# Performance work log

Measured on AMD Instinct MI355X. Metric: run time of the kernel, lower is better.

Reference implementation:

```python
import jax, jax.numpy as jnp
import numpy as np

H, DH, M = 8, 64, 3          # heads, dim_head, num memory tokens
DIM = 512                    # model dim
INNER = H * DH               # 512
SCALE = DH ** -0.5
SQRT_DH = float(np.sqrt(DH))
SQRT_M = float(np.sqrt(M))


def setup_inputs() -> dict:
    key = jax.random.key(0)
    ks = jax.random.split(key, 7)
    b, n = 2, 2048
    x = jax.random.normal(ks[0], (b, n, DIM), dtype=jnp.float32)
    # Linear weights stored as (in, out); y = x @ W
    wq = jax.random.normal(ks[1], (DIM, INNER), dtype=jnp.float32) * (DIM ** -0.5)
    wkv = jax.random.normal(ks[2], (DIM, 2 * INNER), dtype=jnp.float32) * (DIM ** -0.5)
    wo = jax.random.normal(ks[3], (INNER, DIM), dtype=jnp.float32) * (INNER ** -0.5)
    bo = jnp.zeros((DIM,), dtype=jnp.float32)
    # xavier_normal_ std = sqrt(2 / (fan_in + fan_out)) over last two dims (M, INNER)
    xav = float(np.sqrt(2.0 / (M + INNER)))
    m_k = jax.random.normal(ks[4], (1, M, INNER), dtype=jnp.float32) * xav
    m_v = jax.random.normal(ks[5], (1, M, INNER), dtype=jnp.float32) * xav
    return {"x": x, "wq": wq, "wkv": wkv, "wo": wo, "bo": bo, "m_k": m_k, "m_v": m_v}


def reference(x, wq, wkv, wo, bo, m_k, m_v):
    b, n, _ = x.shape
    # projections -> (b, h, n, d)
    q = (x @ wq).reshape(b, n, H, DH).transpose(0, 2, 1, 3)
    kv = x @ wkv
    k, v = jnp.split(kv, 2, axis=-1)
    k = k.reshape(b, n, H, DH).transpose(0, 2, 1, 3)
    v = v.reshape(b, n, H, DH).transpose(0, 2, 1, 3)
    # memory tokens: torch does expand(b, M, INNER).view(b, H, M, DH),
    # a flat reshape (NOT a per-head rearrange) -- replicate exactly.
    mk = SQRT_DH * jnp.broadcast_to(m_k, (b, M, INNER)).reshape(b, H, M, DH)
    mv = SQRT_M * jnp.broadcast_to(m_v, (b, M, INNER)).reshape(b, H, M, DH)
    k = jnp.concatenate([k, mk], axis=2)  # (b, h, n+M, d)
    v = jnp.concatenate([v, mv], axis=2)
    dots = jnp.einsum('bhid,bhjd->bhij', q, k) * SCALE  # (b, h, n, n+M)
    attn = jax.nn.softmax(dots, axis=-1)                # dropout = identity (eval)
    out = jnp.einsum('bhij,bhjd->bhid', attn, v)
    out = out.transpose(0, 2, 1, 3).reshape(b, n, INNER)
    return out @ wo + bo
```

## Files before the change

### kernel.cpp

```cpp
#include <hip/hip_runtime.h>

typedef unsigned short u16;
typedef unsigned int u32;
typedef __attribute__((ext_vector_type(8))) __bf16 bf16x8;
typedef __attribute__((ext_vector_type(4))) float f32x4;

#define DEVI __device__ __forceinline__
#define C1 0.180336880f
#define C2 (-23.0831200f)

DEVI float bf2f(u16 u) {
    unsigned int v = ((unsigned int)u) << 16;
    return __uint_as_float(v);
}
DEVI u16 f2bf(float f) {
    unsigned int x = __float_as_uint(f);
    x += 0x7fffu + ((x >> 16) & 1u);
    return (u16)(x >> 16);
}
DEVI u32 pk2(float lo, float hi) {
    union { __bf16 b[2]; u32 u; } c;
    c.b[0] = (__bf16)lo; c.b[1] = (__bf16)hi;
    return c.u;
}
DEVI bf16x8 ldb8(const u16* p) {
    union { uint4 u; bf16x8 b; } c;
    c.u = *(const uint4*)p;
    return c.b;
}
DEVI f32x4 mfma32(bf16x8 a, bf16x8 b, f32x4 c) {
    return __builtin_amdgcn_mfma_f32_16x16x32_bf16(a, b, c, 0, 0, 0);
}
DEVI float clamp4(float v) { return fminf(fmaxf(v, -1e4f), 1e4f); }
DEVI float fexp2(float x) { return __builtin_amdgcn_exp2f(x); }
DEVI void gld16(const u16* g, u16* l) {
    __builtin_amdgcn_global_load_lds(
        (const __attribute__((address_space(1))) void*)g,
        (__attribute__((address_space(3))) void*)l, 16, 0, 0);
}

__global__ __launch_bounds__(256) void prep(
    const float* __restrict__ wq, const float* __restrict__ wkv,
    const float* __restrict__ wo, const float* __restrict__ x,
    const float* __restrict__ mkf, const float* __restrict__ mvf,
    u16* __restrict__ wqkvT, u16* __restrict__ woT, u16* __restrict__ xb,
    u16* __restrict__ qkv)
{
    const int bid = blockIdx.x, tid = threadIdx.x;
    if (bid < 256) {
        __shared__ u16 T[64][68];
        int j0, k0; const float* W; int ldw; u16* Out;
        if (bid < 192) { int jt = bid % 24, kt = bid / 24;
            j0 = jt * 64; k0 = kt * 64;
            if (j0 < 512) { W = wq + j0;          ldw = 512;  }
            else          { W = wkv + (j0 - 512); ldw = 1024; }
            Out = wqkvT;
        } else { int t = bid - 192;
            j0 = (t >> 3) * 64; k0 = (t & 7) * 64;
            W = wo + j0; ldw = 512; Out = woT;
        }
        const int lr = tid >> 4, lc = tid & 15;
        #pragma unroll
        for (int i = 0; i < 4; ++i) {
            int k = lr + i * 16;
            float4 v = *(const float4*)(W + (size_t)(k0 + k) * ldw + lc * 4);
            u16 p[4] = { f2bf(v.x), f2bf(v.y), f2bf(v.z), f2bf(v.w) };
            *(uint2*)&T[k][lc * 4] = *(uint2*)p;
        }
        __syncthreads();
        #pragma unroll
        for (int i = 0; i < 4; ++i) {
            int j = lr + i * 16;
            u16 p[4];
            #pragma unroll
            for (int c = 0; c < 4; ++c) p[c] = T[lc * 4 + c][j];
            *(uint2*)(Out + (size_t)(j0 + j) * 512 + k0 + lc * 4) = *(uint2*)p;
        }
    } else if (bid < 2304) {
        int e = (bid - 256) * 1024 + tid * 4;
        float4 v = *(const float4*)(x + e);
        u16 p[4] = { f2bf(v.x), f2bf(v.y), f2bf(v.z), f2bf(v.w) };
        *(uint2*)(xb + e) = *(uint2*)p;
    } else {
        int e = (bid - 2304) * 256 + tid;
        int b = e >> 16, rem = e & 65535;
        int row2 = rem >> 10, c = rem & 1023;
        float v = 0.f;
        if (row2 < 3) {
            int hh = (c & 511) >> 6, d = c & 63;
            int src = hh * 192 + row2 * 64 + d;
            v = (c < 512) ? 8.0f * mkf[src] : 1.7320508f * mvf[src];
        }
        qkv[((size_t)b * 2112 + 2048 + row2) * 1536 + 512 + c] = f2bf(v);
    }
}

template<int TM, int TN, bool F32OUT>
__global__ __launch_bounds__(256) void gemmK(
    const u16* __restrict__ A, int lda,
    const u16* __restrict__ BT, int ldb,
    void* __restrict__ Cv, int ldc,
    const float* __restrict__ bias, int K, int mpad)
{
    constexpr int IL = TM / 32, JL = TN / 32;
    __shared__ u16 As0[TM * 32], As1[TM * 32];
    __shared__ u16 Bs0[TN * 32], Bs1[TN * 32];

    const int tid = threadIdx.x;
    const int m0 = blockIdx.x * TM, n0 = blockIdx.y * TN;
    const int w = tid >> 6, lane = tid & 63, l15 = lane & 15, quad = lane >> 4;
    const int wr = w >> 1, wc = w & 1;
    const int sr = lane >> 2, sc = (lane & 3) * 8;

    f32x4 acc[IL][JL];
    #pragma unroll
    for (int i = 0; i < IL; ++i)
        #pragma unroll
        for (int j = 0; j < JL; ++j) acc[i][j] = (f32x4){0.f, 0.f, 0.f, 0.f};

    for (int k0 = 0; k0 < K; k0 += 64) {
        __syncthreads();
        #pragma unroll
        for (int p = 0; p < TM / 64; ++p) {
            int r0 = w * (TM / 4) + p * 16;
            const u16* g = A + (size_t)(m0 + r0 + sr) * lda + k0 + sc;
            gld16(g,      &As0[r0 * 32]);
            gld16(g + 32, &As1[r0 * 32]);
        }
        #pragma unroll
        for (int p = 0; p < TN / 64; ++p) {
            int r0 = w * (TN / 4) + p * 16;
            const u16* g = BT + (size_t)(n0 + r0 + sr) * ldb + k0 + sc;
            gld16(g,      &Bs0[r0 * 32]);
            gld16(g + 32, &Bs1[r0 * 32]);
        }
        __syncthreads();

        #pragma unroll
        for (int ks = 0; ks < 2; ++ks) {
            const u16* Asel = ks ? As1 : As0;
            const u16* Bsel = ks ? Bs1 : Bs0;
            bf16x8 af[IL], bf[JL];
            #pragma unroll
            for (int i = 0; i < IL; ++i)
                af[i] = ldb8(&Asel[(wr * (TM / 2) + 16 * i + l15) * 32 + quad * 8]);
            #pragma unroll
            for (int j = 0; j < JL; ++j)
                bf[j] = ldb8(&Bsel[(wc * (TN / 2) + 16 * j + l15) * 32 + quad * 8]);
            #pragma unroll
            for (int i = 0; i < IL; ++i)
                #pragma unroll
                for (int j = 0; j < JL; ++j)
                    acc[i][j] = mfma32(af[i], bf[j], acc[i][j]);
        }
    }

    #pragma unroll
    for (int j = 0; j < JL; ++j) {
        int col = n0 + wc * (TN / 2) + 16 * j + l15;
        float bv = bias ? bias[col] : 0.f;
        #pragma unroll
        for (int i = 0; i < IL; ++i) {
            #pragma unroll
            for (int r = 0; r < 4; ++r) {
                int row = m0 + wr * (TM / 2) + 16 * i + quad * 4 + r;
                int orow = row + ((row >> 11) * mpad);
                float vr = clamp4(acc[i][j][r] + bv);
                if (F32OUT) ((float*)Cv)[(size_t)orow * ldc + col] = vr;
                else        ((u16*)Cv)[(size_t)orow * ldc + col] = f2bf(vr);
            }
        }
    }
}

__global__ __launch_bounds__(256, 4) void attn_kernel(
    const u16* __restrict__ qkv, u16* __restrict__ Opart,
    float* __restrict__ Lpart)
{
    __shared__ alignas(16) u16 Ks[64][72];
    __shared__ alignas(16) u16 Vt[64][72];
    __shared__ alignas(16) u16 Ps[128][72];

    const int tid = threadIdx.x;
    const int bx = blockIdx.x;
    const int qt = bx >> 2, s = bx & 3;
    const int h = blockIdx.y, b = blockIdx.z;
    const int w = tid >> 6, lane = tid & 63, l15 = lane & 15, quad = lane >> 4;
    const size_t bq = (size_t)b * 2112;
    const int rq = qt * 128;
    const int ro = b * 2048 + qt * 128;

    union { u32 u[4]; bf16x8 b8; } onesu;
    #pragma unroll
    for (int i = 0; i < 4; ++i) onesu.u[i] = 0x3F803F80u;
    const bf16x8 onesf = onesu.b8;

    {
        int row = tid >> 1, cg = (tid & 1) * 32;
        const u16* src = qkv + (bq + rq + row) * 1536 + h * 64 + cg;
        *(uint4*)&Ps[row][cg]      = *(const uint4*)src;
        *(uint4*)&Ps[row][cg + 8]  = *(const uint4*)(src + 8);
        *(uint4*)&Ps[row][cg + 16] = *(const uint4*)(src + 16);
        *(uint4*)&Ps[row][cg + 24] = *(const uint4*)(src + 24);
    }
    __syncthreads();
    bf16x8 qf[2][2];
    #pragma unroll
    for (int sub = 0; sub < 2; ++sub) {
        qf[sub][0] = ldb8(&Ps[64 * sub + 16 * w + l15][quad * 8]);
        qf[sub][1] = ldb8(&Ps[64 * sub + 16 * w + l15][32 + quad * 8]);
    }

    f32x4 Od[2][4], Ol[2];
    #pragma unroll
    for (int sub = 0; sub < 2; ++sub) {
        #pragma unroll
        for (int t = 0; t < 4; ++t) Od[sub][t] = (f32x4){0.f, 0.f, 0.f, 0.f};
        Ol[sub] = (f32x4){0.f, 0.f, 0.f, 0.f};
    }

    const int krow = tid >> 2, kcg = (tid & 3) * 16;
    const int vkp = (tid & 31) * 2, vdg = ((tid >> 5) & 7) * 8;

    const int kt0 = s ? 8 * s + 1 : 0;
    const int kt1 = 8 * s + 9;
    for (int kt = kt0; kt < kt1; ++kt) {
        const u16* ksrc = qkv + (bq + kt * 64 + krow) * 1536 + 512 + h * 64 + kcg;
        uint4 k0 = *(const uint4*)ksrc, k1 = *(const uint4*)(ksrc + 8);
        const u16* vsrc = qkv + (bq + kt * 64 + vkp) * 1536 + 1024 + h * 64 + vdg;
        uint4 v0 = *(const uint4*)vsrc, v1 = *(const uint4*)(vsrc + 1536);
        __syncthreads();
        *(uint4*)&Ks[krow][kcg]     = k0;
        *(uint4*)&Ks[krow][kcg + 8] = k1;
        {
            u32 a0[4] = {v0.x, v0.y, v0.z, v0.w};
            u32 a1[4] = {v1.x, v1.y, v1.z, v1.w};
            #pragma unroll
            for (int i = 0; i < 4; ++i) {
                u32 lo = __builtin_amdgcn_perm(a1[i], a0[i], 0x05040100u);
                u32 hi = __builtin_amdgcn_perm(a1[i], a0[i], 0x07060302u);
                *(u32*)&Vt[vdg + 2 * i][vkp]     = lo;
                *(u32*)&Vt[vdg + 2 * i + 1][vkp] = hi;
            }
        }
        __syncthreads();

        f32x4 d[2][4];
        #pragma unroll
        for (int sub = 0; sub < 2; ++sub)
            #pragma unroll
            for (int t = 0; t < 4; ++t) d[sub][t] = (f32x4){0.f, 0.f, 0.f, 0.f};
        #pragma unroll
        for (int ks = 0; ks < 2; ++ks) {
            #pragma unroll
            for (int t = 0; t < 4; ++t) {
                bf16x8 kf = ldb8(&Ks[16 * t + l15][ks * 32 + quad * 8]);
                d[0][t] = mfma32(kf, qf[0][ks], d[0][t]);
                d[1][t] = mfma32(kf, qf[1][ks], d[1][t]);
            }
        }
        if (kt == 32) {
            #pragma unroll
            for (int sub = 0; sub < 2; ++sub) {
                #pragma unroll
                for (int t = 1; t < 4; ++t)
                    d[sub][t] = (f32x4){-1e9f, -1e9f, -1e9f, -1e9f};
                #pragma unroll
                for (int r = 0; r < 4; ++r)
                    if (!(quad == 0 && r < 3)) d[sub][0][r] = -1e9f;
            }
        }

        #pragma unroll
        for (int sub = 0; sub < 2; ++sub)
            #pragma unroll
            for (int t = 0; t < 4; ++t) {
                uint2 pv = { pk2(fexp2(fmaf(d[sub][t][0], C1, C2)),
                                 fexp2(fmaf(d[sub][t][1], C1, C2))),
                             pk2(fexp2(fmaf(d[sub][t][2], C1, C2)),
                                 fexp2(fmaf(d[sub][t][3], C1, C2))) };
                *(uint2*)&Ps[64 * sub + 16 * w + l15][16 * t + 4 * quad] = pv;
            }
        #pragma unroll
        for (int ks = 0; ks < 2; ++ks) {
            bf16x8 af0 = ldb8(&Ps[16 * w + l15][ks * 32 + quad * 8]);
            bf16x8 af1 = ldb8(&Ps[64 + 16 * w + l15][ks * 32 + quad * 8]);
            #pragma unroll
            for (int dt = 0; dt < 4; ++dt) {
                bf16x8 vf = ldb8(&Vt[16 * dt + l15][ks * 32 + quad * 8]);
                Od[0][dt] = mfma32(af0, vf, Od[0][dt]);
                Od[1][dt] = mfma32(af1, vf, Od[1][dt]);
            }
            Ol[0] = mfma32(af0, onesf, Ol[0]);
            Ol[1] = mfma32(af1, onesf, Ol[1]);
        }
    }

    u16* Ob = Opart + (size_t)s * 4096 * 512;
    #pragma unroll
    for (int sub = 0; sub < 2; ++sub) {
        #pragma unroll
        for (int r = 0; r < 4; ++r) {
            int row = ro + 64 * sub + 16 * w + quad * 4 + r;
            #pragma unroll
            for (int dt = 0; dt < 4; ++dt) {
                int col = h * 64 + 16 * dt + l15;
                Ob[(size_t)row * 512 + col] = f2bf(Od[sub][dt][r]);
            }
            if (l15 == 0)
                Lpart[((size_t)s * 4096 + row) * 8 + h] = Ol[sub][r];
        }
    }
}

__global__ __launch_bounds__(256) void merge_kernel(
    const u16* __restrict__ Opart, const float* __restrict__ Lpart,
    u16* __restrict__ outp)
{
    int e = (blockIdx.x * 256 + threadIdx.x) * 4;
    int row = e >> 9, h = (e & 511) >> 6;
    float ax = 0.f, ay = 0.f, az = 0.f, aw = 0.f, l = 0.f;
    #pragma unroll
    for (int s = 0; s < 4; ++s) {
        uint2 pv = *(const uint2*)(Opart + (size_t)s * 4096 * 512 + e);
        ax += bf2f((u16)(pv.x & 0xffff)); ay += bf2f((u16)(pv.x >> 16));
        az += bf2f((u16)(pv.y & 0xffff)); aw += bf2f((u16)(pv.y >> 16));
        l += Lpart[((size_t)s * 4096 + row) * 8 + h];
    }
    float rl = 1.0f / fmaxf(l, 1e-30f);
    u16 p[4] = { f2bf(clamp4(ax * rl)), f2bf(clamp4(ay * rl)),
                 f2bf(clamp4(az * rl)), f2bf(clamp4(aw * rl)) };
    *(uint2*)(outp + e) = *(uint2*)p;
}

extern "C" void kernel_launch(void* const* d_in, const int* in_sizes, int n_in,
                              void* d_out, int out_size, void* d_ws, size_t ws_size,
                              hipStream_t stream)
{
    (void)in_sizes; (void)n_in; (void)out_size; (void)ws_size;
    const float* x   = (const float*)d_in[0];
    const float* wq  = (const float*)d_in[1];
    const float* wkv = (const float*)d_in[2];
    const float* wo  = (const float*)d_in[3];
    const float* bo  = (const float*)d_in[4];
    const float* mk  = (const float*)d_in[5];
    const float* mv  = (const float*)d_in[6];
    float* out = (float*)d_out;

    u16* qkv   = (u16*)d_ws;
    u16* outp  = qkv + 6488064;
    u16* woT   = outp + 2097152;
    float* Lpart = (float*)(woT + 262144);
    u16* scratch = (u16*)(Lpart + 163840);
    u16* wqkvT = scratch;
    u16* xb    = scratch + 786432;
    u16* Opart = scratch;

    prep<<<2816, 256, 0, stream>>>(wq, wkv, wo, x, mk, mv, wqkvT, woT, xb, qkv);
    gemmK<128, 64, false><<<dim3(32, 24), 256, 0, stream>>>(
        xb, 512, wqkvT, 512, qkv, 1536, nullptr, 512, 64);
    attn_kernel<<<dim3(64, 8, 2), 256, 0, stream>>>(qkv, Opart, Lpart);
    merge_kernel<<<2048, 256, 0, stream>>>(Opart, Lpart, outp);
    gemmK<64, 64, true><<<dim3(64, 8), 256, 0, stream>>>(
        outp, 512, woT, 512, out, 512, bo, 512, 0);
}
```

Before: 129.7 us.

## Fuse split-KV merge into output projection GEMM and enlarge QKV GEMM K-tile

Removes the separate merge kernel: the output-projection GEMM now reads the four split-KV partial outputs and their softmax denominators, sums and normalizes them in registers, and writes the merged bf16 tile straight into shared memory as the A operand. This drops one launch and the write and re-read of the merged intermediate. The cost is that each of the 8 column-blocks repeats the 4-way partial reads and the reduction, which raises Opart traffic. Separately, the QKV GEMM is parameterized on K-tile depth and run with BK=128, halving its barrier iterations at the cost of more shared memory.

```diff
diff --git a/kernel.cpp b/kernel.cpp
--- a/kernel.cpp
+++ b/kernel.cpp
@@ -95,16 +95,16 @@
     }
 }
 
-template<int TM, int TN, bool F32OUT>
+template<int TM, int TN, int BK, bool F32OUT>
 __global__ __launch_bounds__(256) void gemmK(
     const u16* __restrict__ A, int lda,
     const u16* __restrict__ BT, int ldb,
     void* __restrict__ Cv, int ldc,
     const float* __restrict__ bias, int K, int mpad)
 {
-    constexpr int IL = TM / 32, JL = TN / 32;
-    __shared__ u16 As0[TM * 32], As1[TM * 32];
-    __shared__ u16 Bs0[TN * 32], Bs1[TN * 32];
+    constexpr int IL = TM / 32, JL = TN / 32, KS = BK / 32;
+    __shared__ u16 As[KS][TM * 32];
+    __shared__ u16 Bs[KS][TN * 32];
 
     const int tid = threadIdx.x;
     const int m0 = blockIdx.x * TM, n0 = blockIdx.y * TN;
@@ -118,35 +118,35 @@
         #pragma unroll
         for (int j = 0; j < JL; ++j) acc[i][j] = (f32x4){0.f, 0.f, 0.f, 0.f};
 
-    for (int k0 = 0; k0 < K; k0 += 64) {
+    for (int k0 = 0; k0 < K; k0 += BK) {
         __syncthreads();
         #pragma unroll
         for (int p = 0; p < TM / 64; ++p) {
             int r0 = w * (TM / 4) + p * 16;
             const u16* g = A + (size_t)(m0 + r0 + sr) * lda + k0 + sc;
-            gld16(g,      &As0[r0 * 32]);
-            gld16(g + 32, &As1[r0 * 32]);
+            #pragma unroll
+            for (int kk = 0; kk < KS; ++kk)
+                gld16(g + 32 * kk, &As[kk][r0 * 32]);
         }
         #pragma unroll
         for (int p = 0; p < TN / 64; ++p) {
             int r0 = w * (TN / 4) + p * 16;
             const u16* g = BT + (size_t)(n0 + r0 + sr) * ldb + k0 + sc;
-            gld16(g,      &Bs0[r0 * 32]);
-            gld16(g + 32, &Bs1[r0 * 32]);
-        }
-        __syncthreads();
-
-        #pragma unroll
-        for (int ks = 0; ks < 2; ++ks) {
-            const u16* Asel = ks ? As1 : As0;
-            const u16* Bsel = ks ? Bs1 : Bs0;
+            #pragma unroll
+            for (int kk = 0; kk < KS; ++kk)
+                gld16(g + 32 * kk, &Bs[kk][r0 * 32]);
+        }
+        __syncthreads();
+
+        #pragma unroll
+        for (int ks = 0; ks < KS; ++ks) {
             bf16x8 af[IL], bf[JL];
             #pragma unroll
             for (int i = 0; i < IL; ++i)
-                af[i] = ldb8(&Asel[(wr * (TM / 2) + 16 * i + l15) * 32 + quad * 8]);
+                af[i] = ldb8(&As[ks][(wr * (TM / 2) + 16 * i + l15) * 32 + quad * 8]);
             #pragma unroll
             for (int j = 0; j < JL; ++j)
-                bf[j] = ldb8(&Bsel[(wc * (TN / 2) + 16 * j + l15) * 32 + quad * 8]);
+                bf[j] = ldb8(&Bs[ks][(wc * (TN / 2) + 16 * j + l15) * 32 + quad * 8]);
             #pragma unroll
             for (int i = 0; i < IL; ++i)
                 #pragma unroll
@@ -313,24 +313,95 @@
     }
 }
 
-__global__ __launch_bounds__(256) void merge_kernel(
+__global__ __launch_bounds__(256) void gemm2f(
     const u16* __restrict__ Opart, const float* __restrict__ Lpart,
-    u16* __restrict__ outp)
+    const u16* __restrict__ BT, float* __restrict__ Cout,
+    const float* __restrict__ bias)
 {
-    int e = (blockIdx.x * 256 + threadIdx.x) * 4;
-    int row = e >> 9, h = (e & 511) >> 6;
-    float ax = 0.f, ay = 0.f, az = 0.f, aw = 0.f, l = 0.f;
-    #pragma unroll
-    for (int s = 0; s < 4; ++s) {
-        uint2 pv = *(const uint2*)(Opart + (size_t)s * 4096 * 512 + e);
-        ax += bf2f((u16)(pv.x & 0xffff)); ay += bf2f((u16)(pv.x >> 16));
-        az += bf2f((u16)(pv.y & 0xffff)); aw += bf2f((u16)(pv.y >> 16));
-        l += Lpart[((size_t)s * 4096 + row) * 8 + h];
-    }
-    float rl = 1.0f / fmaxf(l, 1e-30f);
-    u16 p[4] = { f2bf(clamp4(ax * rl)), f2bf(clamp4(ay * rl)),
-                 f2bf(clamp4(az * rl)), f2bf(clamp4(aw * rl)) };
-    *(uint2*)(outp + e) = *(uint2*)p;
+    __shared__ u16 As0[64 * 32], As1[64 * 32];
+    __shared__ u16 Bs0[64 * 32], Bs1[64 * 32];
+
+    const int tid = threadIdx.x;
+    const int m0 = blockIdx.x * 64, n0 = blockIdx.y * 64;
+    const int w = tid >> 6, lane = tid & 63, l15 = lane & 15, quad = lane >> 4;
+    const int wr = w >> 1, wc = w & 1;
+    const int sr = lane >> 2, sc = (lane & 3) * 8;
+    const int arow = m0 + w * 16 + sr;
+
+    f32x4 acc[2][2];
+    #pragma unroll
+    for (int i = 0; i < 2; ++i)
+        #pragma unroll
+        for (int j = 0; j < 2; ++j) acc[i][j] = (f32x4){0.f, 0.f, 0.f, 0.f};
+
+    const u16* bG = BT + (size_t)(n0 + w * 16 + sr) * 512 + sc;
+
+    for (int k0 = 0; k0 < 512; k0 += 64) {
+        const int h = k0 >> 6;
+        uint4 oa0[4], oa1[4];
+        float ls = 0.f;
+        #pragma unroll
+        for (int s = 0; s < 4; ++s) {
+            const u16* ob = Opart + ((size_t)s * 4096 + arow) * 512 + k0 + sc;
+            oa0[s] = *(const uint4*)ob;
+            oa1[s] = *(const uint4*)(ob + 32);
+            ls += Lpart[((size_t)s * 4096 + arow) * 8 + h];
+        }
+        float rl = 1.0f / fmaxf(ls, 1e-30f);
+        __syncthreads();
+        gld16(bG + k0,      &Bs0[w * 16 * 32]);
+        gld16(bG + k0 + 32, &Bs1[w * 16 * 32]);
+        #pragma unroll
+        for (int g2 = 0; g2 < 2; ++g2) {
+            u32 pk[4];
+            #pragma unroll
+            for (int e = 0; e < 4; ++e) {
+                float lo = 0.f, hi = 0.f;
+                #pragma unroll
+                for (int s = 0; s < 4; ++s) {
+                    u32 v = g2 ? ((const u32*)&oa1[s])[e] : ((const u32*)&oa0[s])[e];
+                    lo += bf2f((u16)(v & 0xffff));
+                    hi += bf2f((u16)(v >> 16));
+                }
+                pk[e] = pk2(lo * rl, hi * rl);
+            }
+            u16* dst = (g2 ? As1 : As0) + (w * 16 + sr) * 32 + sc;
+            *(uint4*)dst = *(uint4*)pk;
+        }
+        __syncthreads();
+
+        #pragma unroll
+        for (int ks = 0; ks < 2; ++ks) {
+            const u16* Asel = ks ? As1 : As0;
+            const u16* Bsel = ks ? Bs1 : Bs0;
+            bf16x8 af[2], bf[2];
+            #pragma unroll
+            for (int i = 0; i < 2; ++i)
+                af[i] = ldb8(&Asel[(wr * 32 + 16 * i + l15) * 32 + quad * 8]);
+            #pragma unroll
+            for (int j = 0; j < 2; ++j)
+                bf[j] = ldb8(&Bsel[(wc * 32 + 16 * j + l15) * 32 + quad * 8]);
+            #pragma unroll
+            for (int i = 0; i < 2; ++i)
+                #pragma unroll
+                for (int j = 0; j < 2; ++j)
+                    acc[i][j] = mfma32(af[i], bf[j], acc[i][j]);
+        }
+    }
+
+    #pragma unroll
+    for (int j = 0; j < 2; ++j) {
+        int col = n0 + wc * 32 + 16 * j + l15;
+        float bv = bias[col];
+        #pragma unroll
+        for (int i = 0; i < 2; ++i) {
+            #pragma unroll
+            for (int r = 0; r < 4; ++r) {
+                int row = m0 + wr * 32 + 16 * i + quad * 4 + r;
+                Cout[(size_t)row * 512 + col] = clamp4(acc[i][j][r] + bv);
+            }
+        }
+    }
 }
 
 extern "C" void kernel_launch(void* const* d_in, const int* in_sizes, int n_in,
@@ -357,10 +428,8 @@
     u16* Opart = scratch;
 
     prep<<<2816, 256, 0, stream>>>(wq, wkv, wo, x, mk, mv, wqkvT, woT, xb, qkv);
-    gemmK<128, 64, false><<<dim3(32, 24), 256, 0, stream>>>(
+    gemmK<128, 64, 128, false><<<dim3(32, 24), 256, 0, stream>>>(
         xb, 512, wqkvT, 512, qkv, 1536, nullptr, 512, 64);
     attn_kernel<<<dim3(64, 8, 2), 256, 0, stream>>>(qkv, Opart, Lpart);
-    merge_kernel<<<2048, 256, 0, stream>>>(Opart, Lpart, outp);
-    gemmK<64, 64, true><<<dim3(64, 8), 256, 0, stream>>>(
-        outp, 512, woT, 512, out, 512, bo, 512, 0);
-}
+    gemm2f<<<dim3(64, 8), 256, 0, stream>>>(Opart, Lpart, woT, out, bo);
+}
```

Result: no change. 130.0 us (+0.2%).
